# Kernel tuning notes

Measured on AMD Instinct MI355X. Metric: run time of the kernel, lower is better.

## Reference

```python
import jax, jax.numpy as jnp
import numpy as np
import math

FACTOR = 1

def setup_inputs() -> dict:
    key = jax.random.key(0)
    kq, kk, kv = jax.random.split(key, 3)
    B, H, L, E = 8, 8, 1024, 512
    queries = jax.random.normal(kq, (B, H, L, E), dtype=jnp.float32)
    keys = jax.random.normal(kk, (B, H, L, E), dtype=jnp.float32)
    values = jax.random.normal(kv, (B, H, L, E), dtype=jnp.float32)
    return {"queries": queries, "keys": keys, "values": values}

def _time_delay_agg_full(values, corr):
    # values: [B,H,C,Len], corr: [B,H,C,Len]  (C = seq positions, Len = feature dim here)
    length = values.shape[-1]
    top_k = int(FACTOR * math.log(length))
    weights, delay = jax.lax.top_k(corr, top_k)          # [B,H,C,k]
    tmp_corr = jax.nn.softmax(weights, axis=-1)          # [B,H,C,k]
    # gather from values.repeat(...,2) at init_index + delay  ==  circular gather mod length
    idx = (jnp.arange(length)[None, None, None, None, :] + delay[..., None]) % length  # [B,H,C,k,Len]
    gathered = jnp.take_along_axis(values[:, :, :, None, :], idx, axis=-1)             # [B,H,C,k,Len]
    return jnp.einsum('bhckl,bhck->bhcl', gathered, tmp_corr)

def reference(queries, keys, values):
    B, H, L, E = queries.shape
    S = values.shape[2]
    # L == S in this setup, so pad/slice branches are no-ops; keep slice for fidelity
    values = values[:, :, :L, :]
    keys = keys[:, :, :L, :]
    q_fft = jnp.fft.fft(queries, axis=-1)
    k_fft = jnp.fft.fft(keys, axis=-1)
    res = q_fft * jnp.conj(k_fft)
    # torch.fft.irfft(res, n=E) trims the complex input to E//2+1 before inverse; numpy/jax do the same
    corr = jnp.fft.irfft(res, n=E, axis=-1).astype(queries.dtype)  # [B,H,L,E]
    V = _time_delay_agg_full(values, corr)
    return V, jnp.transpose(corr, (0, 3, 1, 2))
```

## Files before the change

kernel.cpp:

```cpp
#include <hip/hip_runtime.h>
#include <math.h>


#define TOPK 6
#define LGKM0 asm volatile("s_waitcnt lgkmcnt(0)" ::: "memory")

__device__ __forceinline__ float2 cmul(float2 a, float2 b) {
  return make_float2(fmaf(a.x, b.x, -(a.y * b.y)), fmaf(a.x, b.y, a.y * b.x));
}
__device__ __forceinline__ float2 cadd(float2 a, float2 b) { return make_float2(a.x + b.x, a.y + b.y); }
__device__ __forceinline__ float2 csub(float2 a, float2 b) { return make_float2(a.x - b.x, a.y - b.y); }
__device__ __forceinline__ float2 mnegi(float2 v) { return make_float2(v.y, -v.x); }

__device__ __forceinline__ unsigned bf16rne(float x) {
  unsigned t = __float_as_uint(x);
  return (t + 0x7FFFu + ((t >> 16) & 1u)) >> 16;
}

__device__ __forceinline__ void radix8(float2 y[8]) {
  float2 p0 = cadd(y[0], y[4]), p1 = csub(y[0], y[4]);
  float2 p2 = cadd(y[2], y[6]), p3 = csub(y[2], y[6]);
  float2 q0 = cadd(y[1], y[5]), q1 = csub(y[1], y[5]);
  float2 q2 = cadd(y[3], y[7]), q3 = csub(y[3], y[7]);
  float2 mp3 = mnegi(p3), mq3 = mnegi(q3);
  float2 E0 = cadd(p0, p2), E2 = csub(p0, p2);
  float2 E1 = cadd(p1, mp3), E3 = csub(p1, mp3);
  float2 O0 = cadd(q0, q2), O2 = csub(q0, q2);
  float2 O1 = cadd(q1, mq3), O3 = csub(q1, mq3);
  const float RT = 0.70710678118654752440f;
  float2 T1 = make_float2(RT * (O1.x + O1.y), RT * (O1.y - O1.x));
  float2 T2 = mnegi(O2);
  float2 T3 = make_float2(RT * (O3.y - O3.x), -RT * (O3.x + O3.y));
  y[0] = cadd(E0, O0); y[4] = csub(E0, O0);
  y[1] = cadd(E1, T1); y[5] = csub(E1, T1);
  y[2] = cadd(E2, T2); y[6] = csub(E2, T2);
  y[3] = cadd(E3, T3); y[7] = csub(E3, T3);
}

__device__ __forceinline__ void twiddle8(float2 y[8], float2 w) {
  float2 wp = w;
  y[1] = cmul(y[1], wp);
  wp = cmul(wp, w); y[2] = cmul(y[2], wp);
  wp = cmul(wp, w); y[3] = cmul(y[3], wp);
  wp = cmul(wp, w); y[4] = cmul(y[4], wp);
  wp = cmul(wp, w); y[5] = cmul(y[5], wp);
  wp = cmul(wp, w); y[6] = cmul(y[6], wp);
  wp = cmul(wp, w); y[7] = cmul(y[7], wp);
}

__device__ __forceinline__ void fft512t(float2 y[8], float* zx, float* zy,
                                        int u, float2 w512u, float2 w64n0) {
  const int f0 = u >> 3, n0 = u & 7;
  radix8(y);
  twiddle8(y, w512u);
#pragma unroll
  for (int r = 0; r < 8; ++r) { int s = 72 * r + u; zx[s] = y[r].x; zy[s] = y[r].y; }
  LGKM0;
#pragma unroll
  for (int j = 0; j < 8; ++j) {
    int s = 72 * f0 + 8 * j + n0;
    y[j] = make_float2(zx[s], zy[s]);
  }
  radix8(y);
  twiddle8(y, w64n0);
  LGKM0;
#pragma unroll
  for (int g = 0; g < 8; ++g) {
    int s = 72 * f0 + 8 * g + (n0 ^ g);
    zx[s] = y[g].x; zy[s] = y[g].y;
  }
  LGKM0;
#pragma unroll
  for (int j = 0; j < 8; ++j) {
    int s = 72 * f0 + 8 * n0 + (j ^ n0);
    y[j] = make_float2(zx[s], zy[s]);
  }
  radix8(y);
}

__global__ __launch_bounds__(512, 4) void autoagg_kernel(
    const float* __restrict__ q, const float* __restrict__ kk,
    const float* __restrict__ v, float* __restrict__ outV,
    float* __restrict__ outC) {
  __shared__ float zscr[8 * 1152];
  __shared__ unsigned short tile[512 * 36];
  const int tid = threadIdx.x;
  const int u = tid & 63;
  const int w = tid >> 6;
  const int bid = blockIdx.x;
  float* zx = zscr + w * 1152;
  float* zy = zx + 576;

  const int f0 = u >> 3, n0 = u & 7;
  const int base = f0 + (n0 << 3);

  const float N2PI = -6.28318530717958647692f;
  float s_, c_;
  __sincosf(N2PI * (float)u * (1.f / 512.f), &s_, &c_);
  const float2 w512u = make_float2(c_, s_);
  __sincosf(N2PI * (float)n0 * (1.f / 64.f), &s_, &c_);
  const float2 w64n0 = make_float2(c_, s_);

#pragma unroll 1
  for (int p = 0; p < 4; ++p) {
    const int row = (bid << 5) + (p << 3) + w;
    const int rowU = __builtin_amdgcn_readfirstlane(row);
    const float* qrow = q + (size_t)rowU * 512;
    const float* krow = kk + (size_t)rowU * 512;
    const float* vrow = v + (size_t)rowU * 512;

    float2 y[8];
#pragma unroll
    for (int m = 0; m < 8; ++m)
      y[m] = make_float2(qrow[u + (m << 6)], krow[u + (m << 6)]);

    fft512t(y, zx, zy, u, w512u, w64n0);

    LGKM0;
#pragma unroll
    for (int r = 0; r < 8; ++r) {
      int s = 72 * r + (n0 << 3) + f0;
      zx[s] = y[r].x; zy[s] = y[r].y;
    }
    LGKM0;
    const float SCL = 1.f / 2048.f;
#pragma unroll
    for (int m = 0; m < 8; ++m) {
      int fA = (m << 6) | u;
      int fB = (512 - fA) & 511;
      int sA = 72 * m + (f0 << 3) + n0;
      int sB = 72 * (fB >> 6) + (((fB >> 3) & 7) << 3) + (fB & 7);
      float Ax = zx[sA], Ay = zy[sA];
      float Bx = zx[sB], By = zy[sB];
      float sx = Ax + Bx, sy = Ay - By;
      float dx = Ax - Bx, dy = Ay + By;
      y[m] = make_float2((sx * dy - sy * dx) * SCL,
                         -fmaf(sx, dx, sy * dy) * SCL);
    }

    fft512t(y, zx, zy, u, w512u, w64n0);

    const int col = (p << 3) | w;
#pragma unroll
    for (int r = 0; r < 8; ++r)
      tile[(base + (r << 6)) * 36 + col] = (unsigned short)bf16rne(y[r].x);

    unsigned key[8];
#pragma unroll
    for (int r = 0; r < 8; ++r) {
      unsigned bb = __float_as_uint(y[r].x);
      unsigned sgn = (unsigned)((int)bb >> 31);
      unsigned mono = bb ^ (sgn | 0x80000000u);
      key[r] = (mono & 0xFFFFFE00u) | (unsigned)(511 - (base + (r << 6)));
    }
    float w0 = 0.f, tw[TOPK]; int dly[TOPK];
#pragma unroll
    for (int it = 0; it < TOPK; ++it) {
      unsigned kmax = key[0];
#pragma unroll
      for (int i = 1; i < 8; ++i) kmax = key[i] > kmax ? key[i] : kmax;
#pragma unroll
      for (int off = 32; off >= 1; off >>= 1) {
        unsigned o = (unsigned)__shfl_xor((int)kmax, off, 64);
        kmax = o > kmax ? o : kmax;
      }
      unsigned mb = kmax & 0xFFFFFE00u;
      unsigned vb = (mb & 0x80000000u) ? (mb ^ 0x80000000u) : ~mb;
      float val = __uint_as_float(vb);
      if (it == 0) w0 = val;
      tw[it] = __expf(val - w0);
      dly[it] = 511 - (int)(kmax & 0x1FFu);
#pragma unroll
      for (int i = 0; i < 8; ++i) if (key[i] == kmax) key[i] = 0u;
    }
    float ssum = 0.f;
#pragma unroll
    for (int it = 0; it < TOPK; ++it) ssum += tw[it];
    const float inv = 1.f / ssum;

    float V[8] = {0.f, 0.f, 0.f, 0.f, 0.f, 0.f, 0.f, 0.f};
#pragma unroll
    for (int it = 0; it < TOPK; ++it) {
      const float twk = tw[it] * inv;
      const int d = dly[it];
#pragma unroll
      for (int i = 0; i < 8; ++i)
        V[i] = fmaf(twk, vrow[(base + (i << 6) + d) & 511], V[i]);
    }

    LGKM0;
#pragma unroll
    for (int i = 0; i < 8; ++i)
      zx[76 * i + 9 * n0 + f0] = V[i];
    LGKM0;
    float vt[8];
#pragma unroll
    for (int j = 0; j < 8; ++j)
      vt[j] = zx[76 * f0 + 9 * n0 + j];
    LGKM0;
    float4* ov = (float4*)(outV + (size_t)rowU * 512 + (u << 3));
    ov[0] = make_float4(vt[0], vt[1], vt[2], vt[3]);
    ov[1] = make_float4(vt[4], vt[5], vt[6], vt[7]);
  }

  __syncthreads();
  const int b9 = bid >> 8;
  const int h9 = (bid >> 5) & 7;
  const int l0 = (bid & 31) << 5;
#pragma unroll
  for (int round = 0; round < 8; ++round) {
    int e = (round << 6) + (tid >> 3);
    int lq = (tid & 7) << 2;
    const unsigned short* tr = tile + e * 36 + lq;
    float4 tv = make_float4(__uint_as_float((unsigned)tr[0] << 16),
                            __uint_as_float((unsigned)tr[1] << 16),
                            __uint_as_float((unsigned)tr[2] << 16),
                            __uint_as_float((unsigned)tr[3] << 16));
    *(float4*)(outC + (((size_t)b9 * 512 + e) * 8 + h9) * 1024 + l0 + lq) = tv;
  }
}

extern "C" void kernel_launch(void* const* d_in, const int* in_sizes, int n_in,
                              void* d_out, int out_size, void* d_ws, size_t ws_size,
                              hipStream_t stream) {
  const float* q = (const float*)d_in[0];
  const float* k = (const float*)d_in[1];
  const float* v = (const float*)d_in[2];
  float* outV = (float*)d_out;
  float* outC = (float*)d_out + (size_t)8 * 8 * 1024 * 512;
  dim3 grid(65536 / 32), block(512);
  hipLaunchKernelGGL(autoagg_kernel, grid, block, 0, stream, q, k, v, outV, outC);
}
```

Baseline: 233.7 us.

## Prefetch next rows, precompute twiddles, use DPP reductions and interleaved LDS

Loads the q/k rows for the next iteration into registers before running the current FFT, so global load latency overlaps with compute. Twiddle powers are computed once per thread instead of in each FFT pass. The wave-wide max in top-k selection uses DPP row ops plus a readlane instead of shfl_xor. LDS scratch is stored as interleaved float2, and the bf16 tile is read back with one 64-bit load. The extra prefetch and twiddle registers raise register pressure against the 4-blocks-per-CU launch bound and could cause spills.

```diff
diff --git a/kernel.cpp b/kernel.cpp
--- a/kernel.cpp
+++ b/kernel.cpp
@@ -15,6 +15,23 @@
 __device__ __forceinline__ unsigned bf16rne(float x) {
   unsigned t = __float_as_uint(x);
   return (t + 0x7FFFu + ((t >> 16) & 1u)) >> 16;
+}
+
+__device__ __forceinline__ unsigned wave_umax64(unsigned x) {
+#define DPPMAX(ctrl)                                                          \
+  {                                                                           \
+    unsigned t = (unsigned)__builtin_amdgcn_update_dpp(0, (int)x, ctrl, 0xf,  \
+                                                       0xf, true);            \
+    x = t > x ? t : x;                                                        \
+  }
+  DPPMAX(0x111)
+  DPPMAX(0x112)
+  DPPMAX(0x114)
+  DPPMAX(0x118)
+  DPPMAX(0x142)
+  DPPMAX(0x143)
+#undef DPPMAX
+  return (unsigned)__builtin_amdgcn_readlane((int)x, 63);
 }
 
 __device__ __forceinline__ void radix8(float2 y[8]) {
@@ -37,44 +54,30 @@
   y[3] = cadd(E3, T3); y[7] = csub(E3, T3);
 }
 
-__device__ __forceinline__ void twiddle8(float2 y[8], float2 w) {
-  float2 wp = w;
-  y[1] = cmul(y[1], wp);
-  wp = cmul(wp, w); y[2] = cmul(y[2], wp);
-  wp = cmul(wp, w); y[3] = cmul(y[3], wp);
-  wp = cmul(wp, w); y[4] = cmul(y[4], wp);
-  wp = cmul(wp, w); y[5] = cmul(y[5], wp);
-  wp = cmul(wp, w); y[6] = cmul(y[6], wp);
-  wp = cmul(wp, w); y[7] = cmul(y[7], wp);
-}
-
-__device__ __forceinline__ void fft512t(float2 y[8], float* zx, float* zy,
-                                        int u, float2 w512u, float2 w64n0) {
+__device__ __forceinline__ void twiddle8p(float2 y[8], const float2 W[7]) {
+#pragma unroll
+  for (int r = 1; r < 8; ++r) y[r] = cmul(y[r], W[r - 1]);
+}
+
+__device__ __forceinline__ void fft512t(float2 y[8], float2* __restrict__ Z,
+                                        int u, const float2 W1[7],
+                                        const float2 W2[7]) {
   const int f0 = u >> 3, n0 = u & 7;
   radix8(y);
-  twiddle8(y, w512u);
-#pragma unroll
-  for (int r = 0; r < 8; ++r) { int s = 72 * r + u; zx[s] = y[r].x; zy[s] = y[r].y; }
+  twiddle8p(y, W1);
+#pragma unroll
+  for (int r = 0; r < 8; ++r) Z[72 * r + u] = y[r];
   LGKM0;
 #pragma unroll
-  for (int j = 0; j < 8; ++j) {
-    int s = 72 * f0 + 8 * j + n0;
-    y[j] = make_float2(zx[s], zy[s]);
-  }
+  for (int j = 0; j < 8; ++j) y[j] = Z[72 * f0 + 8 * j + n0];
   radix8(y);
-  twiddle8(y, w64n0);
+  twiddle8p(y, W2);
   LGKM0;
 #pragma unroll
-  for (int g = 0; g < 8; ++g) {
-    int s = 72 * f0 + 8 * g + (n0 ^ g);
-    zx[s] = y[g].x; zy[s] = y[g].y;
-  }
+  for (int g = 0; g < 8; ++g) Z[72 * f0 + 8 * g + (n0 ^ g)] = y[g];
   LGKM0;
 #pragma unroll
-  for (int j = 0; j < 8; ++j) {
-    int s = 72 * f0 + 8 * n0 + (j ^ n0);
-    y[j] = make_float2(zx[s], zy[s]);
-  }
+  for (int j = 0; j < 8; ++j) y[j] = Z[72 * f0 + 8 * n0 + (j ^ n0)];
   radix8(y);
 }
 
@@ -82,14 +85,14 @@
     const float* __restrict__ q, const float* __restrict__ kk,
     const float* __restrict__ v, float* __restrict__ outV,
     float* __restrict__ outC) {
-  __shared__ float zscr[8 * 1152];
+  __shared__ float2 Zall[8 * 576];
   __shared__ unsigned short tile[512 * 36];
   const int tid = threadIdx.x;
   const int u = tid & 63;
   const int w = tid >> 6;
   const int bid = blockIdx.x;
-  float* zx = zscr + w * 1152;
-  float* zy = zx + 576;
+  float2* Zw = Zall + w * 576;
+  float* zf = (float*)Zw;
 
   const int f0 = u >> 3, n0 = u & 7;
   const int base = f0 + (n0 << 3);
@@ -100,45 +103,63 @@
   const float2 w512u = make_float2(c_, s_);
   __sincosf(N2PI * (float)n0 * (1.f / 64.f), &s_, &c_);
   const float2 w64n0 = make_float2(c_, s_);
+  float2 W1[7], W2[7];
+  {
+    float2 wp = w512u; W1[0] = wp;
+#pragma unroll
+    for (int r = 1; r < 7; ++r) { wp = cmul(wp, w512u); W1[r] = wp; }
+    wp = w64n0; W2[0] = wp;
+#pragma unroll
+    for (int r = 1; r < 7; ++r) { wp = cmul(wp, w64n0); W2[r] = wp; }
+  }
+
+  const int bid5 = bid << 5;
+  float2 pf[8];
+  {
+    const float* qrow = q + (size_t)(bid5 + w) * 512;
+    const float* krow = kk + (size_t)(bid5 + w) * 512;
+#pragma unroll
+    for (int m = 0; m < 8; ++m)
+      pf[m] = make_float2(qrow[u + (m << 6)], krow[u + (m << 6)]);
+  }
 
 #pragma unroll 1
   for (int p = 0; p < 4; ++p) {
-    const int row = (bid << 5) + (p << 3) + w;
-    const int rowU = __builtin_amdgcn_readfirstlane(row);
-    const float* qrow = q + (size_t)rowU * 512;
-    const float* krow = kk + (size_t)rowU * 512;
+    const int rowU = __builtin_amdgcn_readfirstlane(bid5 + (p << 3) + w);
     const float* vrow = v + (size_t)rowU * 512;
 
     float2 y[8];
 #pragma unroll
-    for (int m = 0; m < 8; ++m)
-      y[m] = make_float2(qrow[u + (m << 6)], krow[u + (m << 6)]);
-
-    fft512t(y, zx, zy, u, w512u, w64n0);
-
-    LGKM0;
-#pragma unroll
-    for (int r = 0; r < 8; ++r) {
-      int s = 72 * r + (n0 << 3) + f0;
-      zx[s] = y[r].x; zy[s] = y[r].y;
-    }
+    for (int m = 0; m < 8; ++m) y[m] = pf[m];
+    if (p < 3) {
+      const float* qn = q + (size_t)(rowU + 8) * 512;
+      const float* kn = kk + (size_t)(rowU + 8) * 512;
+#pragma unroll
+      for (int m = 0; m < 8; ++m)
+        pf[m] = make_float2(qn[u + (m << 6)], kn[u + (m << 6)]);
+    }
+
+    fft512t(y, Zw, u, W1, W2);
+
+    LGKM0;
+#pragma unroll
+    for (int r = 0; r < 8; ++r)
+      Zw[72 * r + (n0 << 3) + f0] = y[r];
     LGKM0;
     const float SCL = 1.f / 2048.f;
 #pragma unroll
     for (int m = 0; m < 8; ++m) {
-      int fA = (m << 6) | u;
-      int fB = (512 - fA) & 511;
-      int sA = 72 * m + (f0 << 3) + n0;
+      int fB = (512 - ((m << 6) | u)) & 511;
       int sB = 72 * (fB >> 6) + (((fB >> 3) & 7) << 3) + (fB & 7);
-      float Ax = zx[sA], Ay = zy[sA];
-      float Bx = zx[sB], By = zy[sB];
-      float sx = Ax + Bx, sy = Ay - By;
-      float dx = Ax - Bx, dy = Ay + By;
+      float2 A = Zw[72 * m + (f0 << 3) + n0];
+      float2 Bv = Zw[sB];
+      float sx = A.x + Bv.x, sy = A.y - Bv.y;
+      float dx = A.x - Bv.x, dy = A.y + Bv.y;
       y[m] = make_float2((sx * dy - sy * dx) * SCL,
                          -fmaf(sx, dx, sy * dy) * SCL);
     }
 
-    fft512t(y, zx, zy, u, w512u, w64n0);
+    fft512t(y, Zw, u, W1, W2);
 
     const int col = (p << 3) | w;
 #pragma unroll
@@ -156,14 +177,10 @@
     float w0 = 0.f, tw[TOPK]; int dly[TOPK];
 #pragma unroll
     for (int it = 0; it < TOPK; ++it) {
-      unsigned kmax = key[0];
-#pragma unroll
-      for (int i = 1; i < 8; ++i) kmax = key[i] > kmax ? key[i] : kmax;
-#pragma unroll
-      for (int off = 32; off >= 1; off >>= 1) {
-        unsigned o = (unsigned)__shfl_xor((int)kmax, off, 64);
-        kmax = o > kmax ? o : kmax;
-      }
+      unsigned km = key[0];
+#pragma unroll
+      for (int i = 1; i < 8; ++i) km = key[i] > km ? key[i] : km;
+      unsigned kmax = wave_umax64(km);
       unsigned mb = kmax & 0xFFFFFE00u;
       unsigned vb = (mb & 0x80000000u) ? (mb ^ 0x80000000u) : ~mb;
       float val = __uint_as_float(vb);
@@ -191,12 +208,12 @@
     LGKM0;
 #pragma unroll
     for (int i = 0; i < 8; ++i)
-      zx[76 * i + 9 * n0 + f0] = V[i];
+      zf[76 * i + 9 * n0 + f0] = V[i];
     LGKM0;
     float vt[8];
 #pragma unroll
     for (int j = 0; j < 8; ++j)
-      vt[j] = zx[76 * f0 + 9 * n0 + j];
+      vt[j] = zf[76 * f0 + 9 * n0 + j];
     LGKM0;
     float4* ov = (float4*)(outV + (size_t)rowU * 512 + (u << 3));
     ov[0] = make_float4(vt[0], vt[1], vt[2], vt[3]);
@@ -211,11 +228,11 @@
   for (int round = 0; round < 8; ++round) {
     int e = (round << 6) + (tid >> 3);
     int lq = (tid & 7) << 2;
-    const unsigned short* tr = tile + e * 36 + lq;
-    float4 tv = make_float4(__uint_as_float((unsigned)tr[0] << 16),
-                            __uint_as_float((unsigned)tr[1] << 16),
-                            __uint_as_float((unsigned)tr[2] << 16),
-                            __uint_as_float((unsigned)tr[3] << 16));
+    uint2 tt = *(const uint2*)(tile + e * 36 + lq);
+    float4 tv = make_float4(__uint_as_float(tt.x << 16),
+                            __uint_as_float(tt.x & 0xFFFF0000u),
+                            __uint_as_float(tt.y << 16),
+                            __uint_as_float(tt.y & 0xFFFF0000u));
     *(float4*)(outC + (((size_t)b9 * 512 + e) * 8 + h9) * 1024 + l0 + lq) = tv;
   }
 }
```

Result: slower. 420.9 us (+80.1%).
